# Performance work log

Measured on AMD Instinct MI355X. Metric: run time of the kernel, lower is better.

## Reference

```python
import jax, jax.numpy as jnp
import numpy as np

DIM, HEADS = 512, 8
HD = DIM // HEADS
B, T = 1, 512


def _rope_tables(T, hd):
    inv_freq = 1.0 / (10000.0 ** (jnp.arange(0, hd, 2, dtype=jnp.float32) / hd))
    freqs = jnp.arange(T, dtype=jnp.float32)[:, None] * inv_freq[None, :]
    emb = jnp.concatenate([freqs, freqs], axis=-1)  # [T, hd]
    return jnp.cos(emb), jnp.sin(emb)


def _rotate_half_heads(x):
    # Faithful to source: torch chunk(2, dim=1) on [B,H,hd,1,T] splits the HEADS axis.
    x1, x2 = jnp.split(x, 2, axis=1)
    return jnp.concatenate([-x2, x1], axis=1)


def setup_inputs():
    key = jax.random.key(0)
    ks = jax.random.split(key, 5)
    s = 1.0 / np.sqrt(DIM)
    return {
        "x": jax.random.normal(ks[0], (B, T, DIM), dtype=jnp.float32),
        "Wq": jax.random.normal(ks[1], (DIM, DIM), dtype=jnp.float32) * s,
        "Wk": jax.random.normal(ks[2], (DIM, DIM), dtype=jnp.float32) * s,
        "Wv": jax.random.normal(ks[3], (DIM, DIM), dtype=jnp.float32) * s,
        "Wo": jax.random.normal(ks[4], (DIM, DIM), dtype=jnp.float32) * s,
    }


def reference(x, Wq, Wk, Wv, Wo):
    b, t, d = x.shape
    h, hd = HEADS, d // HEADS
    scale = 1.0 / np.sqrt(hd)

    def proj(W):
        # 1x1 Conv2d == per-position linear; channel o = head*hd + c  -> [B,H,hd,T]
        return jnp.einsum('btd,od->bot', x, W).reshape(b, h, hd, t)

    q, k, v = proj(Wq), proj(Wk), proj(Wv)

    cos, sin = _rope_tables(t, hd)
    cosT = cos.T[None, None]  # [1,1,hd,T]
    sinT = sin.T[None, None]
    q = q * cosT + _rotate_half_heads(q) * sinT
    k = k * cosT + _rotate_half_heads(k) * sinT

    # Per-channel outer-product scores (inner dim of the matmul is the singleton axis)
    att = jnp.einsum('bhci,bhcj->bhcij', q, k) * scale  # [B,H,hd,T,T]
    causal_mask = jnp.triu(jnp.ones((t, t), dtype=bool), k=1)
    att = jnp.where(causal_mask, -jnp.inf, att)
    att = jax.nn.softmax(att, axis=-1)

    out = jnp.einsum('bhcij,bhcj->bhci', att, v).reshape(b, d, t)
    return jnp.einsum('od,bdt->bto', Wo, out)  # [B,T,D]
```

## Files before the change

kernel.cpp:

```cpp
#include <hip/hip_runtime.h>
#include <math.h>

typedef __attribute__((ext_vector_type(8))) short short8;
typedef __attribute__((ext_vector_type(4))) float floatx4;

__device__ __forceinline__ unsigned short f2bf(float f) {
    unsigned int u = __builtin_bit_cast(unsigned int, f);
    u += 0x7FFFu + ((u >> 16) & 1u);
    return (unsigned short)(u >> 16);
}


__global__ __launch_bounds__(256) void cvt_bf16(
    const float* __restrict__ x,  const float* __restrict__ Wq,
    const float* __restrict__ Wk, const float* __restrict__ Wv,
    const float* __restrict__ Wo, unsigned short* __restrict__ Wallb,
    unsigned short* __restrict__ xb, unsigned short* __restrict__ Wob)
{
    const float* src; unsigned short* dst;
    switch (blockIdx.y) {
        case 0: src = Wq; dst = Wallb;          break;
        case 1: src = Wk; dst = Wallb + 262144; break;
        case 2: src = Wv; dst = Wallb + 524288; break;
        case 3: src = x;  dst = xb;             break;
        default: src = Wo; dst = Wob;           break;
    }
    const int i4 = (blockIdx.x * 256 + threadIdx.x) * 4;
    const float4 v = *(const float4*)(src + i4);
    ushort4 o;
    o.x = f2bf(v.x); o.y = f2bf(v.y); o.z = f2bf(v.z); o.w = f2bf(v.w);
    *(ushort4*)(dst + i4) = o;
}

__global__ __launch_bounds__(256) void gemm_bt(
    const unsigned short* __restrict__ A,
    const unsigned short* __restrict__ B,
    float* __restrict__ C)
{
    __shared__ unsigned short As[2][64 * 64];
    __shared__ unsigned short Bs[2][64 * 64];

    const int tid  = threadIdx.x;
    const int lane = tid & 63;
    const int w    = tid >> 6;
    const int m0   = blockIdx.y * 64;
    const int n0   = blockIdx.x * 64;
    const int wm   = (w >> 1) * 32;
    const int wn   = (w & 1) * 32;

    const int srow8 = w * 8 + (lane >> 3);
    const int c8    = lane & 7;

    floatx4 acc[2][2] = {{{0.f,0.f,0.f,0.f},{0.f,0.f,0.f,0.f}},
                         {{0.f,0.f,0.f,0.f},{0.f,0.f,0.f,0.f}}};

    const int quad = lane >> 4;
    const int l15  = lane & 15;

    auto stage = [&](int kc, int buf) {
        #pragma unroll
        for (int rr = 0; rr < 2; ++rr) {
            const int row  = rr * 32 + srow8;
            const int gcol = kc + ((c8 ^ (row & 7)) * 8);
            const unsigned short* ga = A + (m0 + row) * 512 + gcol;
            const unsigned short* gb = B + (n0 + row) * 512 + gcol;
            __builtin_amdgcn_global_load_lds(
                (const __attribute__((address_space(1))) void*)ga,
                (__attribute__((address_space(3))) void*)&As[buf][(rr * 32 + w * 8) * 64],
                16, 0, 0);
            __builtin_amdgcn_global_load_lds(
                (const __attribute__((address_space(1))) void*)gb,
                (__attribute__((address_space(3))) void*)&Bs[buf][(rr * 32 + w * 8) * 64],
                16, 0, 0);
        }
    };

    stage(0, 0);

    #pragma unroll
    for (int kt = 0; kt < 8; ++kt) {
        const int cur = kt & 1;
        if (kt < 7) {
            stage((kt + 1) * 64, cur ^ 1);
            asm volatile("s_waitcnt vmcnt(4)" ::: "memory");
        } else {
            asm volatile("s_waitcnt vmcnt(0)" ::: "memory");
        }
        __builtin_amdgcn_s_barrier();
        __builtin_amdgcn_sched_barrier(0);

        #pragma unroll
        for (int ks = 0; ks < 2; ++ks) {
            const int cIdx = ks * 4 + quad;
            short8 a[2], b[2];
            #pragma unroll
            for (int mt = 0; mt < 2; ++mt) {
                const int row = wm + mt * 16 + l15;
                a[mt] = *(const short8*)&As[cur][row * 64 + ((cIdx ^ (row & 7)) * 8)];
            }
            #pragma unroll
            for (int nt = 0; nt < 2; ++nt) {
                const int row = wn + nt * 16 + l15;
                b[nt] = *(const short8*)&Bs[cur][row * 64 + ((cIdx ^ (row & 7)) * 8)];
            }
            #pragma unroll
            for (int mt = 0; mt < 2; ++mt)
                #pragma unroll
                for (int nt = 0; nt < 2; ++nt)
                    acc[mt][nt] = __builtin_amdgcn_mfma_f32_16x16x32_bf16(
                        a[mt], b[nt], acc[mt][nt], 0, 0, 0);
        }
        __builtin_amdgcn_s_barrier();
        __builtin_amdgcn_sched_barrier(0);
    }

    #pragma unroll
    for (int mt = 0; mt < 2; ++mt)
        #pragma unroll
        for (int nt = 0; nt < 2; ++nt) {
            const int grow = m0 + wm + mt * 16 + quad * 4;
            const int gcol = n0 + wn + nt * 16 + l15;
            #pragma unroll
            for (int r = 0; r < 4; ++r)
                C[(grow + r) * 512 + gcol] = acc[mt][nt][r];
        }
}

__global__ __launch_bounds__(256) void attn_rope(
    const float* __restrict__ qkv, unsigned short* __restrict__ attTb)
{
    const int ch = blockIdx.x;
    const int t  = threadIdx.x;
    const int i1 = t;
    const int i2 = 511 - t;
    const int p  = ch ^ 256;
    const float sgn = (ch < 256) ? -1.f : 1.f;

    __shared__ float ks_[512];
    __shared__ float vs_[512];

    const float* __restrict__ qg = qkv;
    const float* __restrict__ kg = qkv + 262144;
    const float* __restrict__ vg = qkv + 524288;

    const float inv_freq = powf(10000.f, -(float)(ch & 31) * (1.f / 32.f));
    const float SC = 0.125f * 1.44269504088896f;

    float sn_a, cs_a, sn_b, cs_b, sn_c, cs_c;
    sincosf((float)t * inv_freq,         &sn_a, &cs_a);
    sincosf((float)(t + 256) * inv_freq, &sn_b, &cs_b);
    sincosf((float)i2 * inv_freq,        &sn_c, &cs_c);

    ks_[t]       = (kg[ch * 512 + t]       * cs_a + sgn * kg[p * 512 + t]       * sn_a) * SC;
    ks_[t + 256] = (kg[ch * 512 + t + 256] * cs_b + sgn * kg[p * 512 + t + 256] * sn_b) * SC;
    vs_[t]       = vg[ch * 512 + t];
    vs_[t + 256] = vg[ch * 512 + t + 256];
    const float q1 = qg[ch * 512 + i1] * cs_a + sgn * qg[p * 512 + i1] * sn_a;
    const float q2 = qg[ch * 512 + i2] * cs_c + sgn * qg[p * 512 + i2] * sn_c;
    __syncthreads();

    float l1 = 0.f, a1 = 0.f, l2 = 0.f, a2 = 0.f;
    const int w64 = t & ~63;

    #pragma unroll 2
    for (int j = 0; j < w64; j += 4) {
        const float4 kk = *(const float4*)&ks_[j];
        const float4 vv = *(const float4*)&vs_[j];
        float e;
        e = __builtin_amdgcn_exp2f(q1 * kk.x); l1 += e; a1 = fmaf(e, vv.x, a1);
        e = __builtin_amdgcn_exp2f(q2 * kk.x); l2 += e; a2 = fmaf(e, vv.x, a2);
        e = __builtin_amdgcn_exp2f(q1 * kk.y); l1 += e; a1 = fmaf(e, vv.y, a1);
        e = __builtin_amdgcn_exp2f(q2 * kk.y); l2 += e; a2 = fmaf(e, vv.y, a2);
        e = __builtin_amdgcn_exp2f(q1 * kk.z); l1 += e; a1 = fmaf(e, vv.z, a1);
        e = __builtin_amdgcn_exp2f(q2 * kk.z); l2 += e; a2 = fmaf(e, vv.z, a2);
        e = __builtin_amdgcn_exp2f(q1 * kk.w); l1 += e; a1 = fmaf(e, vv.w, a1);
        e = __builtin_amdgcn_exp2f(q2 * kk.w); l2 += e; a2 = fmaf(e, vv.w, a2);
    }
    #pragma unroll 4
    for (int u = 0; u < 64; u += 4) {
        const int j = w64 + u;
        const float4 kk = *(const float4*)&ks_[j];
        const float4 vv = *(const float4*)&vs_[j];
        float e;
        e = (j + 0 <= i1) ? __builtin_amdgcn_exp2f(q1 * kk.x) : 0.f; l1 += e; a1 = fmaf(e, vv.x, a1);
        e = __builtin_amdgcn_exp2f(q2 * kk.x);                       l2 += e; a2 = fmaf(e, vv.x, a2);
        e = (j + 1 <= i1) ? __builtin_amdgcn_exp2f(q1 * kk.y) : 0.f; l1 += e; a1 = fmaf(e, vv.y, a1);
        e = __builtin_amdgcn_exp2f(q2 * kk.y);                       l2 += e; a2 = fmaf(e, vv.y, a2);
        e = (j + 2 <= i1) ? __builtin_amdgcn_exp2f(q1 * kk.z) : 0.f; l1 += e; a1 = fmaf(e, vv.z, a1);
        e = __builtin_amdgcn_exp2f(q2 * kk.z);                       l2 += e; a2 = fmaf(e, vv.z, a2);
        e = (j + 3 <= i1) ? __builtin_amdgcn_exp2f(q1 * kk.w) : 0.f; l1 += e; a1 = fmaf(e, vv.w, a1);
        e = __builtin_amdgcn_exp2f(q2 * kk.w);                       l2 += e; a2 = fmaf(e, vv.w, a2);
    }
    const int jend2 = 448 - w64;
    #pragma unroll 2
    for (int j = w64 + 64; j < jend2; j += 4) {
        const float4 kk = *(const float4*)&ks_[j];
        const float4 vv = *(const float4*)&vs_[j];
        float e;
        e = __builtin_amdgcn_exp2f(q2 * kk.x); l2 += e; a2 = fmaf(e, vv.x, a2);
        e = __builtin_amdgcn_exp2f(q2 * kk.y); l2 += e; a2 = fmaf(e, vv.y, a2);
        e = __builtin_amdgcn_exp2f(q2 * kk.z); l2 += e; a2 = fmaf(e, vv.z, a2);
        e = __builtin_amdgcn_exp2f(q2 * kk.w); l2 += e; a2 = fmaf(e, vv.w, a2);
    }
    #pragma unroll 4
    for (int u = 0; u < 64; u += 4) {
        const int j = jend2 + u;
        const float4 kk = *(const float4*)&ks_[j];
        const float4 vv = *(const float4*)&vs_[j];
        float e;
        e = (j + 0 <= i2) ? __builtin_amdgcn_exp2f(q2 * kk.x) : 0.f; l2 += e; a2 = fmaf(e, vv.x, a2);
        e = (j + 1 <= i2) ? __builtin_amdgcn_exp2f(q2 * kk.y) : 0.f; l2 += e; a2 = fmaf(e, vv.y, a2);
        e = (j + 2 <= i2) ? __builtin_amdgcn_exp2f(q2 * kk.z) : 0.f; l2 += e; a2 = fmaf(e, vv.z, a2);
        e = (j + 3 <= i2) ? __builtin_amdgcn_exp2f(q2 * kk.w) : 0.f; l2 += e; a2 = fmaf(e, vv.w, a2);
    }

    attTb[i1 * 512 + ch] = f2bf(a1 / l1);
    attTb[i2 * 512 + ch] = f2bf(a2 / l2);
}

extern "C" void kernel_launch(void* const* d_in, const int* in_sizes, int n_in,
                              void* d_out, int out_size, void* d_ws, size_t ws_size,
                              hipStream_t stream)
{
    const float* x  = (const float*)d_in[0];
    const float* Wq = (const float*)d_in[1];
    const float* Wk = (const float*)d_in[2];
    const float* Wv = (const float*)d_in[3];
    const float* Wo = (const float*)d_in[4];
    float* out = (float*)d_out;

    unsigned short* Wallb = (unsigned short*)d_ws;
    unsigned short* xb    = Wallb + 786432;
    unsigned short* Wob   = xb + 262144;
    unsigned short* attTb = Wob + 262144;
    float* qkvf = (float*)(attTb + 262144);

    cvt_bf16<<<dim3(256, 5), 256, 0, stream>>>(x, Wq, Wk, Wv, Wo, Wallb, xb, Wob);
    gemm_bt<<<dim3(8, 24), 256, 0, stream>>>(Wallb, xb, qkvf);
    attn_rope<<<512, 256, 0, stream>>>(qkvf, attTb);
    gemm_bt<<<dim3(8, 8), 256, 0, stream>>>(attTb, Wob, out);
}
```

Baseline: 93.68 us.

## Load full K panel into LDS once instead of double-buffered K tiles

The GEMM kernel now loads the entire 64x512 A and B panels into shared memory up front with one wait and barrier, then runs all K steps from LDS without per-step barriers. This removes the per-iteration synchronization and staging overhead. In exchange it needs 128 KB of LDS per block, which limits occupancy to one block per CU (or may exceed limits), and it gives up overlap between loads and MFMA compute.

Result: no change. 92.75 us (-1.0%).

```diff
diff --git a/kernel.cpp b/kernel.cpp
--- a/kernel.cpp
+++ b/kernel.cpp
@@ -37,8 +37,8 @@
     const unsigned short* __restrict__ B,
     float* __restrict__ C)
 {
-    __shared__ unsigned short As[2][64 * 64];
-    __shared__ unsigned short Bs[2][64 * 64];
+    __shared__ unsigned short As[64 * 512];
+    __shared__ unsigned short Bs[64 * 512];
 
     const int tid  = threadIdx.x;
     const int lane = tid & 63;
@@ -48,60 +48,45 @@
     const int wm   = (w >> 1) * 32;
     const int wn   = (w & 1) * 32;
 
-    const int srow8 = w * 8 + (lane >> 3);
-    const int c8    = lane & 7;
-
     floatx4 acc[2][2] = {{{0.f,0.f,0.f,0.f},{0.f,0.f,0.f,0.f}},
                          {{0.f,0.f,0.f,0.f},{0.f,0.f,0.f,0.f}}};
 
     const int quad = lane >> 4;
     const int l15  = lane & 15;
 
-    auto stage = [&](int kc, int buf) {
-        #pragma unroll
-        for (int rr = 0; rr < 2; ++rr) {
-            const int row  = rr * 32 + srow8;
-            const int gcol = kc + ((c8 ^ (row & 7)) * 8);
-            const unsigned short* ga = A + (m0 + row) * 512 + gcol;
-            const unsigned short* gb = B + (n0 + row) * 512 + gcol;
-            __builtin_amdgcn_global_load_lds(
-                (const __attribute__((address_space(1))) void*)ga,
-                (__attribute__((address_space(3))) void*)&As[buf][(rr * 32 + w * 8) * 64],
-                16, 0, 0);
-            __builtin_amdgcn_global_load_lds(
-                (const __attribute__((address_space(1))) void*)gb,
-                (__attribute__((address_space(3))) void*)&Bs[buf][(rr * 32 + w * 8) * 64],
-                16, 0, 0);
-        }
-    };
-
-    stage(0, 0);
+    #pragma unroll
+    for (int r = 0; r < 16; ++r) {
+        const int row = w * 16 + r;
+        const int col = (lane ^ (row & 7)) * 8;
+        __builtin_amdgcn_global_load_lds(
+            (const __attribute__((address_space(1))) void*)(A + (m0 + row) * 512 + col),
+            (__attribute__((address_space(3))) void*)&As[row * 512],
+            16, 0, 0);
+        __builtin_amdgcn_global_load_lds(
+            (const __attribute__((address_space(1))) void*)(B + (n0 + row) * 512 + col),
+            (__attribute__((address_space(3))) void*)&Bs[row * 512],
+            16, 0, 0);
+    }
+
+    asm volatile("s_waitcnt vmcnt(0)" ::: "memory");
+    __builtin_amdgcn_s_barrier();
+    __builtin_amdgcn_sched_barrier(0);
 
     #pragma unroll
     for (int kt = 0; kt < 8; ++kt) {
-        const int cur = kt & 1;
-        if (kt < 7) {
-            stage((kt + 1) * 64, cur ^ 1);
-            asm volatile("s_waitcnt vmcnt(4)" ::: "memory");
-        } else {
-            asm volatile("s_waitcnt vmcnt(0)" ::: "memory");
-        }
-        __builtin_amdgcn_s_barrier();
-        __builtin_amdgcn_sched_barrier(0);
-
         #pragma unroll
         for (int ks = 0; ks < 2; ++ks) {
-            const int cIdx = ks * 4 + quad;
+            const int cIdx = kt * 8 + ks * 4 + quad;
             short8 a[2], b[2];
             #pragma unroll
             for (int mt = 0; mt < 2; ++mt) {
                 const int row = wm + mt * 16 + l15;
-                a[mt] = *(const short8*)&As[cur][row * 64 + ((cIdx ^ (row & 7)) * 8)];
+                a[mt] = *(const short8*)&As[row * 512 + ((cIdx ^ (row & 7)) * 8)];
             }
             #pragma unroll
             for (int nt = 0; nt < 2; ++nt) {
                 const int row = wn + nt * 16 + l15;
-                b[nt] = *(const short8*)&Bs[cur][row * 64 + ((cIdx ^ (row & 7)) * 8)];
+                b[nt] = *(const short8*)&Bs[row * 512 + ((cIdx ^ (row & 7)) * 8)];
             }
             #pragma unroll
             for (int mt = 0; mt < 2; ++mt)
@@ -110,8 +95,6 @@
                     acc[mt][nt] = __builtin_amdgcn_mfma_f32_16x16x32_bf16(
                         a[mt], b[nt], acc[mt][nt], 0, 0, 0);
         }
-        __builtin_amdgcn_s_barrier();
-        __builtin_amdgcn_sched_barrier(0);
     }
 
     #pragma unroll
```
